# Kernel optimization log

Measured on AMD Instinct MI355X. Metric: run time of the kernel, lower is better.

## Reference

```python
import jax, jax.numpy as jnp
import numpy as np

ROUTINGS = 3
EPS = 1e-9

def _squash(s):
    # squash along the capsule-vector (last) axis
    sq = jnp.sum(s * s, axis=-1, keepdims=True)
    return s * (sq / (1.0 + sq)) / jnp.sqrt(sq + EPS)

def setup_inputs() -> dict:
    key = jax.random.key(0)
    k1, k2 = jax.random.split(key)
    B, N, D, d = 32, 64, 128, 128  # batch, num_capsule(=input_num_capsule), dim_capsule, input_dim_capsule
    x = jax.random.normal(k1, (B, N, d), dtype=jnp.float32)
    W = jax.random.normal(k2, (1, N, N, D, d), dtype=jnp.float32)
    return {"x": x, "W": W}

def reference(x, W):
    # u[b,j,k,:] = W[0,j,k] @ x[b,j]  (faithful to broadcast matmul, N==I)
    u = jnp.einsum('jkde,bje->bjkd', W[0], x)  # (B,N,N,D)
    b = jnp.zeros_like(u)                      # routing logits carry D axis per source
    v = None
    for i in range(ROUTINGS):
        c = jax.nn.softmax(b, axis=2)
        s = jnp.sum(c * u, axis=1, keepdims=True)  # (B,1,N,D)
        v = _squash(s)
        if i < ROUTINGS - 1:
            b = b + u * v  # (inputs*outputs).sum over trailing singleton dim
    return v[:, 0, :, :, None]  # (B,N,D,1) matching torch outputs.squeeze(1)
```

## Files before the change

kernel.cpp:

```cpp
#include <hip/hip_runtime.h>

#define NB 32
#define NN 64
#define ND 128
#define NE 128
#define NK 64

typedef float  f32x4  __attribute__((ext_vector_type(4)));
typedef short  short8 __attribute__((ext_vector_type(8)));
typedef __bf16 bf16x8 __attribute__((ext_vector_type(8)));

union Frag { bf16x8 h; short8 s; };

static constexpr size_t UT_BYTES = (size_t)NB * NN * NN * ND * 2;
static constexpr size_t U_BYTES  = (size_t)NB * NN * ND * NK * 2;
static constexpr size_t V_BYTES  = (size_t)NB * ND * NK * 4;
static constexpr size_t WS_NEED  = UT_BYTES + U_BYTES + 2 * V_BYTES;

#define GLOAD16(g, l)                                                   \
    __builtin_amdgcn_global_load_lds(                                   \
        (const __attribute__((address_space(1))) void*)(g),             \
        (__attribute__((address_space(3))) void*)(l), 16, 0, 0)

template <int CTRL, int RMASK>
__device__ __forceinline__ float dppf(float x) {
    int xi = __float_as_int(x);
    return __int_as_float(__builtin_amdgcn_update_dpp(xi, xi, CTRL, RMASK, 0xF, false));
}
__device__ __forceinline__ float wave_sum(float x) {
    x += dppf<0xB1, 0xF>(x);
    x += dppf<0x4E, 0xF>(x);
    x += dppf<0x141, 0xF>(x);
    x += dppf<0x140, 0xF>(x);
    x += dppf<0x142, 0xA>(x);
    x += dppf<0x143, 0xC>(x);
    return __int_as_float(__builtin_amdgcn_readlane(__float_as_int(x), 63));
}

__device__ __forceinline__ ushort f2bf(float f) {
    __bf16 h = (__bf16)f;
    ushort r;
    __builtin_memcpy(&r, &h, 2);
    return r;
}
__device__ __forceinline__ float bf2f(ushort r) {
    return __int_as_float(((int)r) << 16);
}
__device__ __forceinline__ void cvt8f(const f32x4& a, const f32x4& b, Frag& fr) {
    fr.h[0] = (__bf16)a[0]; fr.h[1] = (__bf16)a[1]; fr.h[2] = (__bf16)a[2]; fr.h[3] = (__bf16)a[3];
    fr.h[4] = (__bf16)b[0]; fr.h[5] = (__bf16)b[1]; fr.h[6] = (__bf16)b[2]; fr.h[7] = (__bf16)b[3];
}

__global__ __launch_bounds__(256, 2) void k_u(const float* __restrict__ W,
                                              const float* __restrict__ x,
                                              ushort* __restrict__ u_tmp) {
    struct WaveSh {
        union {
            float  w[2][2048];
            ushort t[32][132];
        };
    };
    __shared__ WaveSh sh[4];

    const int t  = threadIdx.x;
    const int wv = t >> 6;
    const int l  = t & 63;
    const int gw = blockIdx.x * 4 + wv;
    const int j  = gw >> 6;
    const int k  = gw & 63;

    const int lr = l & 15;
    const int lh = l >> 4;

    const float* xb = x + (size_t)j * NE;
    f32x4 xf[2][4][2];
#pragma unroll
    for (int mt = 0; mt < 2; ++mt)
#pragma unroll
        for (int ec = 0; ec < 4; ++ec) {
            const float* p = xb + (size_t)(mt * 16 + lr) * (NN * NE) + ec * 32 + lh * 8;
            xf[mt][ec][0] = *reinterpret_cast<const f32x4*>(p);
            xf[mt][ec][1] = *reinterpret_cast<const f32x4*>(p + 4);
        }
    asm volatile("s_waitcnt vmcnt(0)" ::: "memory");
    __builtin_amdgcn_sched_barrier(0);
    Frag a[2][4];
#pragma unroll
    for (int mt = 0; mt < 2; ++mt)
#pragma unroll
        for (int ec = 0; ec < 4; ++ec) cvt8f(xf[mt][ec][0], xf[mt][ec][1], a[mt][ec]);

    const char* Wg = (const char*)W + ((size_t)(j * NN + k) * ND) * (NE * 4);
#define STAGE(c, buf)                                                         \
    {                                                                         \
        _Pragma("unroll") for (int i_ = 0; i_ < 8; ++i_) {                    \
            const int rl_ = 2 * i_ + (l >> 5);                                \
            const char* gp_ = Wg + ((size_t)((c) * 16 + rl_) << 9) +          \
                              (((l & 31) ^ (rl_ & 7)) << 4);                  \
            GLOAD16(gp_, &sh[wv].w[buf][i_ * 256]);                           \
        }                                                                     \
    }

    STAGE(0, 0);
    STAGE(1, 1);

    f32x4 acc[2][8];
#pragma unroll
    for (int mt = 0; mt < 2; ++mt)
#pragma unroll
        for (int nt = 0; nt < 8; ++nt) acc[mt][nt] = (f32x4)0.0f;

#pragma unroll
    for (int c = 0; c < 8; ++c) {
        const int buf = c & 1;
        if (c < 7) { asm volatile("s_waitcnt vmcnt(8)" ::: "memory"); }
        else       { asm volatile("s_waitcnt vmcnt(0)" ::: "memory"); }
        __builtin_amdgcn_sched_barrier(0);

        const char* cb = (const char*)&sh[wv].w[buf][0] + lr * 512;
        f32x4 g[4][2];
#pragma unroll
        for (int ec = 0; ec < 4; ++ec)
#pragma unroll
            for (int h = 0; h < 2; ++h) {
                const int pos = (ec * 8 + lh * 2 + h) ^ (lr & 7);
                g[ec][h] = *reinterpret_cast<const f32x4*>(cb + pos * 16);
            }
        asm volatile("s_waitcnt lgkmcnt(0)" ::: "memory");
        __builtin_amdgcn_sched_barrier(0);
        if (c < 6) STAGE(c + 2, buf);

#pragma unroll
        for (int ec = 0; ec < 4; ++ec) {
            Frag bw;
            cvt8f(g[ec][0], g[ec][1], bw);
#pragma unroll
            for (int mt = 0; mt < 2; ++mt)
                acc[mt][c] = __builtin_amdgcn_mfma_f32_16x16x32_bf16(
                    a[mt][ec].s, bw.s, acc[mt][c], 0, 0, 0);
        }
    }
#undef STAGE

#pragma unroll
    for (int mt = 0; mt < 2; ++mt)
#pragma unroll
        for (int nt = 0; nt < 8; ++nt)
#pragma unroll
            for (int r = 0; r < 4; ++r)
                sh[wv].t[mt * 16 + lh * 4 + r][nt * 16 + lr] = f2bf(acc[mt][nt][r]);
    asm volatile("s_waitcnt lgkmcnt(0)" ::: "memory");
    __builtin_amdgcn_sched_barrier(0);

#pragma unroll
    for (int i = 0; i < 8; ++i) {
        const int b  = i * 4 + (l >> 4);
        const int d0 = (l & 15) * 8;
        short8 v = *reinterpret_cast<const short8*>(&sh[wv].t[b][d0]);
        ushort* up = u_tmp + (((size_t)b * NN + j) * NK + k) * ND + d0;
        *reinterpret_cast<short8*>(up) = v;
    }
}

__global__ __launch_bounds__(256) void k_t(const ushort* __restrict__ u_tmp,
                                           ushort* __restrict__ u) {
    __shared__ ushort Lt[64][136];
    const int bj = blockIdx.x;
    const int b  = bj >> 6;
    const int j  = bj & 63;
    const int t  = threadIdx.x;

    const ushort* src = u_tmp + ((size_t)(b * NN + j) * NK) * ND;
#pragma unroll
    for (int q = 0; q < 4; ++q) {
        const int flat = q * 256 + t;
        const int k    = flat >> 4;
        const int gcol = flat & 15;
        short8 v = *reinterpret_cast<const short8*>(src + (size_t)k * ND + gcol * 8);
        *reinterpret_cast<short8*>(&Lt[k][gcol * 8]) = v;
    }
    __syncthreads();

    ushort* dst = u + ((size_t)(b * NN + j) * ND) * NK;
#pragma unroll
    for (int q = 0; q < 4; ++q) {
        const int flat = q * 256 + t;
        const int kg   = flat >> 7;
        const int d    = flat & 127;
        short8 v;
#pragma unroll
        for (int r = 0; r < 8; ++r) v[r] = (short)Lt[kg * 8 + r][d];
        *reinterpret_cast<short8*>(dst + (size_t)d * NK + kg * 8) = v;
    }
}

__global__ __launch_bounds__(512) void k_route(const ushort* __restrict__ u,
                                               const float* __restrict__ Vsum,
                                               float* __restrict__ s,
                                               int first) {
    __shared__ float P[8][8][65];
    const int b  = blockIdx.x >> 4;
    const int dg = blockIdx.x & 15;
    const int t  = threadIdx.x;
    const int wv = t >> 6;
    const int l  = t & 63;

    float sacc[8];
#pragma unroll
    for (int dd = 0; dd < 8; ++dd) sacc[dd] = 0.0f;

    const ushort* ub = u + (((size_t)b * NN + wv * 8) * ND + dg * 8) * NK + l;

    if (first) {
        for (int jj = 0; jj < 8; ++jj) {
            const ushort* up = ub + (size_t)jj * (ND * NK);
#pragma unroll
            for (int dd = 0; dd < 8; ++dd) sacc[dd] += bf2f(up[dd * NK]);
        }
#pragma unroll
        for (int dd = 0; dd < 8; ++dd) sacc[dd] *= (1.0f / 64.0f);
    } else {
        float vs[8];
#pragma unroll
        for (int dd = 0; dd < 8; ++dd)
            vs[dd] = Vsum[((size_t)b * ND + dg * 8 + dd) * NK + l];

        for (int jj = 0; jj < 8; ++jj) {
            const ushort* up = ub + (size_t)jj * (ND * NK);
            float uv[8];
#pragma unroll
            for (int dd = 0; dd < 8; ++dd) uv[dd] = bf2f(up[dd * NK]);
#pragma unroll
            for (int dd = 0; dd < 8; ++dd) {
                float p = __expf(uv[dd] * vs[dd] - 32.0f);
                float q = wave_sum(p);
                sacc[dd] = fmaf(p * __builtin_amdgcn_rcpf(q), uv[dd], sacc[dd]);
            }
        }
    }

#pragma unroll
    for (int dd = 0; dd < 8; ++dd) P[wv][dd][l] = sacc[dd];
    __syncthreads();

    const int dd = t >> 6;
    const int k  = t & 63;
    float r = P[0][dd][k];
#pragma unroll
    for (int w2 = 1; w2 < 8; ++w2) r += P[w2][dd][k];
    s[((size_t)b * ND + dg * 8 + dd) * NK + k] = r;
}

__global__ __launch_bounds__(256) void k_squash(const float* __restrict__ s,
                                                float* __restrict__ Vsum,
                                                float* __restrict__ out,
                                                int mode) {
    const int t  = threadIdx.x;
    const int gw = blockIdx.x * 4 + (t >> 6);
    const int b  = gw >> 6;
    const int k  = gw & 63;
    const int l  = t & 63;

    const float s0 = s[((size_t)b * ND + l) * NK + k];
    const float s1 = s[((size_t)b * ND + l + 64) * NK + k];
    float sq    = wave_sum(fmaf(s0, s0, s1 * s1));
    float scale = (sq / (1.0f + sq)) * rsqrtf(sq + 1e-9f);
    float v0 = s0 * scale, v1 = s1 * scale;
    if (mode == 2) {
        float* op = out + ((size_t)b * NN + k) * ND;
        op[l]      = v0;
        op[l + 64] = v1;
    } else if (mode == 0) {
        float* vp = Vsum + (size_t)b * ND * NK + k;
        vp[(size_t)l * NK]        = v0;
        vp[(size_t)(l + 64) * NK] = v1;
    } else {
        float* vp = Vsum + (size_t)b * ND * NK + k;
        vp[(size_t)l * NK]        += v0;
        vp[(size_t)(l + 64) * NK] += v1;
    }
}

extern "C" void kernel_launch(void* const* d_in, const int* in_sizes, int n_in,
                              void* d_out, int out_size, void* d_ws, size_t ws_size,
                              hipStream_t stream) {
    (void)in_sizes; (void)n_in; (void)out_size;
    const float* x = (const float*)d_in[0];
    const float* W = (const float*)d_in[1];
    float* out = (float*)d_out;

    if (ws_size < WS_NEED) return;
    char* ws = (char*)d_ws;
    ushort* u_tmp = (ushort*)ws;
    ushort* u     = (ushort*)(ws + UT_BYTES);
    float* Vsum   = (float*)(ws + UT_BYTES + U_BYTES);
    float* s      = (float*)(ws + UT_BYTES + U_BYTES + V_BYTES);

    k_u<<<dim3(1024), dim3(256), 0, stream>>>(W, x, u_tmp);
    k_t<<<dim3(2048), dim3(256), 0, stream>>>(u_tmp, u);
    for (int it = 0; it < 3; ++it) {
        k_route<<<dim3(512), dim3(512), 0, stream>>>(u, Vsum, s, it == 0 ? 1 : 0);
        k_squash<<<dim3(512), dim3(256), 0, stream>>>(s, Vsum, out, it);
    }
}
```

Measured before the change: 137.8 us.

## Reorganize u layouts and remap k_u work to per-chunk waves with direct stores

k_u now assigns each wave a strided set of 16-row W chunks across all k for a given j. It writes each 16x32 tile straight to u_tmp in a (j,k,d,b) layout, dropping the LDS staging transpose at the end. k_t is rewritten to transpose per (j, d-quarter) block with a swizzled LDS buffer into a new (j,d,b,k) layout for u, and k_route's indexing is updated to match. This aims to raise occupancy and cut LDS use in k_u and to improve coalescing in the transpose, at the cost of narrower 8-byte global stores and larger strides in k_route's reads.

```diff
diff --git a/kernel.cpp b/kernel.cpp
--- a/kernel.cpp
+++ b/kernel.cpp
@@ -12,8 +12,8 @@
 
 union Frag { bf16x8 h; short8 s; };
 
-static constexpr size_t UT_BYTES = (size_t)NB * NN * NN * ND * 2;
-static constexpr size_t U_BYTES  = (size_t)NB * NN * ND * NK * 2;
+static constexpr size_t UT_BYTES = (size_t)NN * NN * ND * NB * 2;
+static constexpr size_t U_BYTES  = (size_t)NN * ND * NB * NK * 2;
 static constexpr size_t V_BYTES  = (size_t)NB * ND * NK * 4;
 static constexpr size_t WS_NEED  = UT_BYTES + U_BYTES + 2 * V_BYTES;
 
@@ -54,20 +54,13 @@
 __global__ __launch_bounds__(256, 2) void k_u(const float* __restrict__ W,
                                               const float* __restrict__ x,
                                               ushort* __restrict__ u_tmp) {
-    struct WaveSh {
-        union {
-            float  w[2][2048];
-            ushort t[32][132];
-        };
-    };
-    __shared__ WaveSh sh[4];
-
+    __shared__ float Wl[4][2][2048];
     const int t  = threadIdx.x;
     const int wv = t >> 6;
     const int l  = t & 63;
-    const int gw = blockIdx.x * 4 + wv;
-    const int j  = gw >> 6;
-    const int k  = gw & 63;
+    const int g  = blockIdx.x * 4 + wv;
+    const int j  = g >> 5;
+    const int w  = g & 31;
 
     const int lr = l & 15;
     const int lh = l >> 4;
@@ -90,107 +83,98 @@
 #pragma unroll
         for (int ec = 0; ec < 4; ++ec) cvt8f(xf[mt][ec][0], xf[mt][ec][1], a[mt][ec]);
 
-    const char* Wg = (const char*)W + ((size_t)(j * NN + k) * ND) * (NE * 4);
-#define STAGE(c, buf)                                                         \
-    {                                                                         \
-        _Pragma("unroll") for (int i_ = 0; i_ < 8; ++i_) {                    \
-            const int rl_ = 2 * i_ + (l >> 5);                                \
-            const char* gp_ = Wg + ((size_t)((c) * 16 + rl_) << 9) +          \
-                              (((l & 31) ^ (rl_ & 7)) << 4);                  \
-            GLOAD16(gp_, &sh[wv].w[buf][i_ * 256]);                           \
-        }                                                                     \
+#define STAGE(ci, buf)                                                         \
+    {                                                                          \
+        const int c_ = (ci) * 32 + w;                                          \
+        const char* base_ = (const char*)W +                                   \
+            (((size_t)(j * NN + (c_ >> 3)) * ND + (c_ & 7) * 16) * NE) * 4;    \
+        _Pragma("unroll") for (int i_ = 0; i_ < 8; ++i_) {                     \
+            const int rl_ = 2 * i_ + (l >> 5);                                 \
+            GLOAD16(base_ + rl_ * 512 + (((l & 31) ^ (rl_ & 7)) << 4),         \
+                    &Wl[wv][buf][i_ * 256]);                                   \
+        }                                                                      \
     }
 
     STAGE(0, 0);
     STAGE(1, 1);
 
-    f32x4 acc[2][8];
-#pragma unroll
-    for (int mt = 0; mt < 2; ++mt)
-#pragma unroll
-        for (int nt = 0; nt < 8; ++nt) acc[mt][nt] = (f32x4)0.0f;
-
-#pragma unroll
-    for (int c = 0; c < 8; ++c) {
-        const int buf = c & 1;
-        if (c < 7) { asm volatile("s_waitcnt vmcnt(8)" ::: "memory"); }
-        else       { asm volatile("s_waitcnt vmcnt(0)" ::: "memory"); }
+#pragma unroll
+    for (int i = 0; i < 16; ++i) {
+        if (i == 0)      { asm volatile("s_waitcnt vmcnt(8)" ::: "memory"); }
+        else if (i < 15) { asm volatile("s_waitcnt vmcnt(10)" ::: "memory"); }
+        else             { asm volatile("s_waitcnt vmcnt(4)" ::: "memory"); }
         __builtin_amdgcn_sched_barrier(0);
 
-        const char* cb = (const char*)&sh[wv].w[buf][0] + lr * 512;
-        f32x4 g[4][2];
+        const char* cb = (const char*)&Wl[wv][i & 1][0];
+        f32x4 gq[4][2];
 #pragma unroll
         for (int ec = 0; ec < 4; ++ec)
 #pragma unroll
             for (int h = 0; h < 2; ++h) {
                 const int pos = (ec * 8 + lh * 2 + h) ^ (lr & 7);
-                g[ec][h] = *reinterpret_cast<const f32x4*>(cb + pos * 16);
+                gq[ec][h] = *reinterpret_cast<const f32x4*>(cb + lr * 512 + pos * 16);
             }
         asm volatile("s_waitcnt lgkmcnt(0)" ::: "memory");
         __builtin_amdgcn_sched_barrier(0);
-        if (c < 6) STAGE(c + 2, buf);
-
+        if (i < 14) STAGE(i + 2, i & 1);
+
+        f32x4 acc0 = (f32x4)0.0f, acc1 = (f32x4)0.0f;
 #pragma unroll
         for (int ec = 0; ec < 4; ++ec) {
             Frag bw;
-            cvt8f(g[ec][0], g[ec][1], bw);
-#pragma unroll
-            for (int mt = 0; mt < 2; ++mt)
-                acc[mt][c] = __builtin_amdgcn_mfma_f32_16x16x32_bf16(
-                    a[mt][ec].s, bw.s, acc[mt][c], 0, 0, 0);
-        }
+            cvt8f(gq[ec][0], gq[ec][1], bw);
+            acc0 = __builtin_amdgcn_mfma_f32_16x16x32_bf16(a[0][ec].s, bw.s, acc0, 0, 0, 0);
+            acc1 = __builtin_amdgcn_mfma_f32_16x16x32_bf16(a[1][ec].s, bw.s, acc1, 0, 0, 0);
+        }
+
+        const int c  = i * 32 + w;
+        char* op = (char*)u_tmp +
+                   (((size_t)(j * NN + (c >> 3)) * ND + (c & 7) * 16) * NB) * 2;
+        uint2 pv0, pv1;
+        pv0.x = (uint)f2bf(acc0[0]) | ((uint)f2bf(acc0[1]) << 16);
+        pv0.y = (uint)f2bf(acc0[2]) | ((uint)f2bf(acc0[3]) << 16);
+        pv1.x = (uint)f2bf(acc1[0]) | ((uint)f2bf(acc1[1]) << 16);
+        pv1.y = (uint)f2bf(acc1[2]) | ((uint)f2bf(acc1[3]) << 16);
+        *reinterpret_cast<uint2*>(op + lr * 64 + lh * 8)      = pv0;
+        *reinterpret_cast<uint2*>(op + lr * 64 + 32 + lh * 8) = pv1;
     }
 #undef STAGE
-
-#pragma unroll
-    for (int mt = 0; mt < 2; ++mt)
-#pragma unroll
-        for (int nt = 0; nt < 8; ++nt)
-#pragma unroll
-            for (int r = 0; r < 4; ++r)
-                sh[wv].t[mt * 16 + lh * 4 + r][nt * 16 + lr] = f2bf(acc[mt][nt][r]);
-    asm volatile("s_waitcnt lgkmcnt(0)" ::: "memory");
-    __builtin_amdgcn_sched_barrier(0);
-
-#pragma unroll
-    for (int i = 0; i < 8; ++i) {
-        const int b  = i * 4 + (l >> 4);
-        const int d0 = (l & 15) * 8;
-        short8 v = *reinterpret_cast<const short8*>(&sh[wv].t[b][d0]);
-        ushort* up = u_tmp + (((size_t)b * NN + j) * NK + k) * ND + d0;
-        *reinterpret_cast<short8*>(up) = v;
-    }
-}
-
-__global__ __launch_bounds__(256) void k_t(const ushort* __restrict__ u_tmp,
-                                           ushort* __restrict__ u) {
-    __shared__ ushort Lt[64][136];
-    const int bj = blockIdx.x;
-    const int b  = bj >> 6;
-    const int j  = bj & 63;
-    const int t  = threadIdx.x;
-
-    const ushort* src = u_tmp + ((size_t)(b * NN + j) * NK) * ND;
-#pragma unroll
-    for (int q = 0; q < 4; ++q) {
-        const int flat = q * 256 + t;
-        const int k    = flat >> 4;
-        const int gcol = flat & 15;
-        short8 v = *reinterpret_cast<const short8*>(src + (size_t)k * ND + gcol * 8);
-        *reinterpret_cast<short8*>(&Lt[k][gcol * 8]) = v;
+}
+
+__global__ __launch_bounds__(256, 2) void k_t(const ushort* __restrict__ u_tmp,
+                                              ushort* __restrict__ u) {
+    __shared__ ushort Lt[NN * 512];
+    const int j  = blockIdx.x >> 3;
+    const int dq = blockIdx.x & 7;
+    const int t  = threadIdx.x;
+    const int l  = t & 63;
+
+#pragma unroll
+    for (int it = 0; it < 16; ++it) {
+        const int k   = it * 4 + (t >> 6);
+        const int swz = (k ^ (k >> 3)) & 7;
+        short8 v = *reinterpret_cast<const short8*>(
+            u_tmp + ((size_t)(j * NN + k) * ND + dq * 16) * NB + l * 8);
+        *reinterpret_cast<short8*>(&Lt[k * 512 + ((l ^ swz) * 8)]) = v;
     }
     __syncthreads();
 
-    ushort* dst = u + ((size_t)(b * NN + j) * ND) * NK;
-#pragma unroll
-    for (int q = 0; q < 4; ++q) {
-        const int flat = q * 256 + t;
-        const int kg   = flat >> 7;
-        const int d    = flat & 127;
+#pragma unroll
+    for (int it = 0; it < 16; ++it) {
+        const int p  = it * 256 + t;
+        const int kg = p & 7;
+        const int b  = (p >> 3) & 31;
+        const int dd = p >> 8;
         short8 v;
 #pragma unroll
-        for (int r = 0; r < 8; ++r) v[r] = (short)Lt[kg * 8 + r][d];
-        *reinterpret_cast<short8*>(dst + (size_t)d * NK + kg * 8) = v;
+        for (int r = 0; r < 8; ++r) {
+            const int k   = kg * 8 + r;
+            const int swz = (k ^ (k >> 3)) & 7;
+            const int G   = dd * 4 + (b >> 3);
+            v[r] = (short)Lt[k * 512 + ((G ^ swz) * 8) + (b & 7)];
+        }
+        *reinterpret_cast<short8*>(
+            u + ((size_t)(j * ND + dq * 16 + dd) * NB + b) * NK + kg * 8) = v;
     }
 }
 
@@ -209,13 +193,15 @@
 #pragma unroll
     for (int dd = 0; dd < 8; ++dd) sacc[dd] = 0.0f;
 
-    const ushort* ub = u + (((size_t)b * NN + wv * 8) * ND + dg * 8) * NK + l;
+    const size_t JS = (size_t)ND * NB * NK;
+    const ushort* ub = u + ((size_t)(wv * 8) * ND + dg * 8) * (NB * NK) +
+                       (size_t)b * NK + l;
 
     if (first) {
         for (int jj = 0; jj < 8; ++jj) {
-            const ushort* up = ub + (size_t)jj * (ND * NK);
-#pragma unroll
-            for (int dd = 0; dd < 8; ++dd) sacc[dd] += bf2f(up[dd * NK]);
+            const ushort* up = ub + jj * JS;
+#pragma unroll
+            for (int dd = 0; dd < 8; ++dd) sacc[dd] += bf2f(up[dd * (NB * NK)]);
         }
 #pragma unroll
         for (int dd = 0; dd < 8; ++dd) sacc[dd] *= (1.0f / 64.0f);
@@ -226,10 +212,10 @@
             vs[dd] = Vsum[((size_t)b * ND + dg * 8 + dd) * NK + l];
 
         for (int jj = 0; jj < 8; ++jj) {
-            const ushort* up = ub + (size_t)jj * (ND * NK);
+            const ushort* up = ub + jj * JS;
             float uv[8];
 #pragma unroll
-            for (int dd = 0; dd < 8; ++dd) uv[dd] = bf2f(up[dd * NK]);
+            for (int dd = 0; dd < 8; ++dd) uv[dd] = bf2f(up[dd * (NB * NK)]);
 #pragma unroll
             for (int dd = 0; dd < 8; ++dd) {
                 float p = __expf(uv[dd] * vs[dd] - 32.0f);
@@ -296,8 +282,8 @@
     float* Vsum   = (float*)(ws + UT_BYTES + U_BYTES);
     float* s      = (float*)(ws + UT_BYTES + U_BYTES + V_BYTES);
 
-    k_u<<<dim3(1024), dim3(256), 0, stream>>>(W, x, u_tmp);
-    k_t<<<dim3(2048), dim3(256), 0, stream>>>(u_tmp, u);
+    k_u<<<dim3(512), dim3(256), 0, stream>>>(W, x, u_tmp);
+    k_t<<<dim3(512), dim3(256), 0, stream>>>(u_tmp, u);
     for (int it = 0; it < 3; ++it) {
         k_route<<<dim3(512), dim3(512), 0, stream>>>(u, Vsum, s, it == 0 ? 1 : 0);
         k_squash<<<dim3(512), dim3(256), 0, stream>>>(s, Vsum, out, it);
```

Result: faster. 131.9 us (-4.2%).
